# Optimization experiments

Hardware: AMD Instinct MI355X
Metric: run time of the kernel (lower is better)

## Reference

```python
import jax, jax.numpy as jnp
import numpy as np

D_MODEL = 1024
N_HEAD = 16
DH = D_MODEL // N_HEAD


def setup_inputs() -> dict:
    key = jax.random.key(0)
    ks = jax.random.split(key, 5)
    B, T = 4, 2048
    scale = 0.02
    return {
        "x": jax.random.normal(ks[0], (B, T, D_MODEL), dtype=jnp.float32),
        "Wqkv": jax.random.normal(ks[1], (D_MODEL, 3 * D_MODEL), dtype=jnp.float32) * scale,
        "bqkv": jnp.zeros((3 * D_MODEL,), dtype=jnp.float32),
        "Wout": jax.random.normal(ks[2], (D_MODEL, D_MODEL), dtype=jnp.float32) * scale,
        "bout": jnp.zeros((D_MODEL,), dtype=jnp.float32),
    }


def reference(x, Wqkv, bqkv, Wout, bout):
    B, T, C = x.shape
    qkv = x @ Wqkv + bqkv  # [B,T,3C]
    q, k, v = jnp.split(qkv, 3, axis=2)
    # [B,T,C] -> [B,H,T,dh]
    def heads(t):
        return t.reshape(B, T, N_HEAD, DH).transpose(0, 2, 1, 3)
    q, k, v = heads(q), heads(k), heads(v)
    scores = jnp.einsum("bhqd,bhkd->bhqk", q, k) / jnp.sqrt(jnp.float32(DH))
    causal = jnp.tril(jnp.ones((T, T), dtype=bool))  # [T,T]
    neg = jnp.finfo(scores.dtype).min
    scores = jnp.where(causal[None, None, :, :], scores, neg)
    A = jax.nn.softmax(scores, axis=-1)
    y = jnp.einsum("bhqk,bhkd->bhqd", A, v)
    y = y.transpose(0, 2, 1, 3).reshape(B, T, C)
    return y @ Wout + bout
```

## Files before the change

### kernel.cpp

```cpp
#include <hip/hip_runtime.h>
#include <hip/hip_bf16.h>

typedef float f32x4 __attribute__((ext_vector_type(4)));
typedef float f32x16 __attribute__((ext_vector_type(16)));
typedef short s16x8 __attribute__((ext_vector_type(8)));
typedef short s16x4 __attribute__((ext_vector_type(4)));
typedef unsigned int u32x4 __attribute__((ext_vector_type(4)));

#define B_ 4
#define T_ 2048
#define C_ 1024
#define H_ 16
#define DH_ 64
#define M_ (B_*T_)
#define N3_ (3*C_)

static __device__ __forceinline__ short f2bf(float f) {
    __hip_bfloat16 h = __float2bfloat16(f);
    return *reinterpret_cast<short*>(&h);
}

static __device__ __forceinline__ unsigned pack2(float lo, float hi) {
    unsigned r;
    asm("v_cvt_pk_bf16_f32 %0, %1, %2" : "=v"(r) : "v"(lo), "v"(hi));
    return r;
}

static __device__ __forceinline__ float exp2_raw(float x) {
    float r;
    asm("v_exp_f32 %0, %1" : "=v"(r) : "v"(x));
    return r;
}

static __device__ __forceinline__ void gload16(const void* g, void* l) {
    __builtin_amdgcn_global_load_lds(
        (const __attribute__((address_space(1))) void*)g,
        (__attribute__((address_space(3))) void*)l, 16, 0, 0);
}

static __device__ __forceinline__ s16x8 lds_frag(const short* base, int row, int chunk) {
    return *(const s16x8*)&base[(row << 6) + ((chunk ^ (row & 7)) << 3)];
}


__global__ __launch_bounds__(256) void cast_f32_bf16(
    const float* __restrict__ in, short* __restrict__ out, int n8)
{
    int i = blockIdx.x * 256 + threadIdx.x;
    if (i >= n8) return;
    float4 a = *(const float4*)&in[i * 8];
    float4 b = *(const float4*)&in[i * 8 + 4];
    s16x8 o = { f2bf(a.x), f2bf(a.y), f2bf(a.z), f2bf(a.w),
                f2bf(b.x), f2bf(b.y), f2bf(b.z), f2bf(b.w) };
    *(s16x8*)&out[i * 8] = o;
}

__global__ __launch_bounds__(256) void transpose_cast(
    const float* __restrict__ src, short* __restrict__ dst, int K, int N)
{
    __shared__ short t[64][66];
    int tid = threadIdx.x;
    int n0 = blockIdx.x * 64, k0 = blockIdx.y * 64;
    #pragma unroll
    for (int p = 0; p < 4; ++p) {
        int cid = tid + p * 256;
        int r = cid >> 4, c4 = cid & 15;
        float4 v = *(const float4*)&src[(size_t)(k0 + r) * N + n0 + c4 * 4];
        t[r][c4 * 4 + 0] = f2bf(v.x);
        t[r][c4 * 4 + 1] = f2bf(v.y);
        t[r][c4 * 4 + 2] = f2bf(v.z);
        t[r][c4 * 4 + 3] = f2bf(v.w);
    }
    __syncthreads();
    #pragma unroll
    for (int p = 0; p < 4; ++p) {
        int cid = tid + p * 256;
        int r = cid >> 4, c4 = cid & 15;
        s16x4 ov;
        #pragma unroll
        for (int j = 0; j < 4; ++j) ov[j] = t[c4 * 4 + j][r];
        *(s16x4*)&dst[(size_t)(n0 + r) * K + k0 + c4 * 4] = ov;
    }
}


template<int MODE>
__global__ __launch_bounds__(256) void gemm_bt(
    const short* __restrict__ A, const short* __restrict__ Bt,
    const float* __restrict__ bias, float* __restrict__ out,
    short* __restrict__ qout, short* __restrict__ kout, short* __restrict__ vout)
{
    const int K = 1024;
    __shared__ short As[128 * 64];
    __shared__ short Bs[128 * 64];
    int tid = threadIdx.x;
    int lane = tid & 63, w = tid >> 6;
    int d = lane & 15, g = lane >> 4;
    int wm = w >> 1, wn = w & 1;

    int gx = gridDim.x;
    int lid = blockIdx.y * gx + blockIdx.x;
    int chunk = (gx * gridDim.y) >> 3;
    int sl = (lid & 7) * chunk + (lid >> 3);
    int m0 = (sl / gx) * 128, n0 = (sl % gx) * 128;

    f32x4 acc[4][4];
    #pragma unroll
    for (int i = 0; i < 4; ++i)
        #pragma unroll
        for (int j = 0; j < 4; ++j) acc[i][j] = (f32x4){0.f, 0.f, 0.f, 0.f};

    for (int kt = 0; kt < K; kt += 64) {
        #pragma unroll
        for (int p = 0; p < 4; ++p) {
            int cid = p * 256 + tid;
            int r = cid >> 3, c8 = cid & 7;
            int co = (c8 ^ (r & 7)) << 3;
            int dofs = (p * 256 + (tid & ~63)) * 8;
            gload16(&A[(size_t)(m0 + r) * K + kt + co], &As[dofs]);
            gload16(&Bt[(size_t)(n0 + r) * K + kt + co], &Bs[dofs]);
        }
        __syncthreads();
        #pragma unroll
        for (int ks = 0; ks < 2; ++ks) {
            s16x8 af[4], bf[4];
            #pragma unroll
            for (int i = 0; i < 4; ++i) {
                af[i] = lds_frag(As, wm * 64 + i * 16 + d, ks * 4 + g);
                bf[i] = lds_frag(Bs, wn * 64 + i * 16 + d, ks * 4 + g);
            }
            #pragma unroll
            for (int mi = 0; mi < 4; ++mi)
                #pragma unroll
                for (int ni = 0; ni < 4; ++ni)
                    acc[mi][ni] = __builtin_amdgcn_mfma_f32_16x16x32_bf16(
                        af[mi], bf[ni], acc[mi][ni], 0, 0, 0);
        }
        __syncthreads();
    }

    #pragma unroll
    for (int mi = 0; mi < 4; ++mi)
        #pragma unroll
        for (int ni = 0; ni < 4; ++ni) {
            int gn = n0 + wn * 64 + ni * 16 + d;
            float bv = bias[gn];
            int gm0 = m0 + wm * 64 + mi * 16 + g * 4;
            if (MODE == 0) {
                #pragma unroll
                for (int r = 0; r < 4; ++r)
                    out[(size_t)(gm0 + r) * 1024 + gn] = acc[mi][ni][r] + bv;
            } else {
                int which = gn >> 10, cc = gn & 1023;
                int h = cc >> 6, dh = cc & 63;
                int b = gm0 >> 11;
                if (which == 2) {
                    int g2 = ((g & 1) << 1) | (g >> 1);
                    int t0v = (gm0 & 2047) - g * 4 + g2 * 4;
                    s16x4 pv;
                    #pragma unroll
                    for (int r = 0; r < 4; ++r) pv[r] = f2bf(acc[mi][ni][r] + bv);
                    *(s16x4*)&vout[((size_t)(b * 16 + h) * 64 + dh) * 2048 + t0v] = pv;
                } else if (which == 1) {
                    int t0 = gm0 & 2047;
                    #pragma unroll
                    for (int r = 0; r < 4; ++r)
                        kout[((size_t)(b * 16 + h) * 2048 + (t0 + r)) * 64 + dh] =
                            f2bf(acc[mi][ni][r] + bv);
                } else {
                    int t0 = gm0 & 2047;
                    const float SC2 = 0.125f * 1.44269504089f;
                    #pragma unroll
                    for (int r = 0; r < 4; ++r)
                        qout[((size_t)(b * 16 + h) * 2048 + (t0 + r)) * 64 + dh] =
                            f2bf((acc[mi][ni][r] + bv) * SC2);
                }
            }
        }
}


__global__ __launch_bounds__(256, 4) void attn_fwd(
    const short* __restrict__ q, const short* __restrict__ kk,
    const short* __restrict__ vt, short* __restrict__ y)
{
    __shared__ short Ks[2][64 * 64];
    __shared__ short Vs[2][64 * 64];
    int tid = threadIdx.x, w = tid >> 6;
    int lane = tid & 63;
    int q5 = lane & 31, h5 = lane >> 5;
    int bid = blockIdx.x;
    int idx = bid >> 3;
    int qt = 15 - (idx >> 3);
    int bh = ((idx & 7) << 3) | (bid & 7);
    int b = bh >> 4, hh = bh & 15;
    const size_t hb = (size_t)bh * 2048 * 64;
    int nt = 2 * qt + 2;
    int qrow = qt * 128 + w * 32;
    int qg = qrow + q5;

    s16x8 qf[4];
    #pragma unroll
    for (int s = 0; s < 4; ++s)
        qf[s] = *(const s16x8*)&q[hb + (size_t)qg * 64 + 16 * s + 8 * h5];

    f32x16 oA, oB;
    #pragma unroll
    for (int i = 0; i < 16; ++i) { oA[i] = 0.f; oB[i] = 0.f; }
    float l = 0.f;

    #define STAGE(buf, kt2) do { \
        _Pragma("unroll") \
        for (int p = 0; p < 2; ++p) { \
            int cid = p * 256 + tid; \
            int r__ = cid >> 3, c8__ = cid & 7; \
            int co__ = (c8__ ^ (r__ & 7)) << 3; \
            int dofs__ = (p * 256 + (tid & ~63)) * 8; \
            gload16(&kk[hb + (size_t)((kt2) * 64 + r__) * 64 + co__], &Ks[buf][dofs__]); \
            gload16(&vt[hb + (size_t)r__ * 2048 + (kt2) * 64 + co__], &Vs[buf][dofs__]); \
        } \
    } while (0)

    STAGE(0, 0);
    int cur = 0;

    #pragma unroll 1
    for (int t = 0; t < nt; ++t) {
        if (t + 1 < nt) {
            STAGE(cur ^ 1, t + 1);
            asm volatile("s_waitcnt vmcnt(4)" ::: "memory");
        } else {
            asm volatile("s_waitcnt vmcnt(0)" ::: "memory");
        }
        __builtin_amdgcn_s_barrier();

        if (t * 64 <= qrow + 31) {
            const short* Kb = Ks[cur];
            const short* Vb = Vs[cur];

            f32x16 sA, sB;
            #pragma unroll
            for (int i = 0; i < 16; ++i) { sA[i] = 0.f; sB[i] = 0.f; }
            #pragma unroll
            for (int s = 0; s < 4; ++s) {
                sA = __builtin_amdgcn_mfma_f32_32x32x16_bf16(
                    lds_frag(Kb, q5, 2 * s + h5), qf[s], sA, 0, 0, 0);
                sB = __builtin_amdgcn_mfma_f32_32x32x16_bf16(
                    lds_frag(Kb, 32 + q5, 2 * s + h5), qf[s], sB, 0, 0, 0);
            }

            float eA[16], eB[16];
            float S = 0.f;
            if (t * 64 + 63 > qrow) {
                #pragma unroll
                for (int rg = 0; rg < 16; ++rg) {
                    int kg = t * 64 + (rg & 3) + 8 * (rg >> 2) + 4 * h5;
                    float a = exp2_raw(sA[rg]); if (kg > qg) a = 0.f;
                    float c = exp2_raw(sB[rg]); if (kg + 32 > qg) c = 0.f;
                    eA[rg] = a; eB[rg] = c; S += a + c;
                }
            } else {
                #pragma unroll
                for (int rg = 0; rg < 16; ++rg) {
                    float a = exp2_raw(sA[rg]);
                    float c = exp2_raw(sB[rg]);
                    eA[rg] = a; eB[rg] = c; S += a + c;
                }
            }
            l += S;

            unsigned wdA[8], wdB[8];
            #pragma unroll
            for (int m = 0; m < 4; ++m) {
                wdA[2 * m]     = pack2(eA[4 * m],     eA[4 * m + 1]);
                wdA[2 * m + 1] = pack2(eA[4 * m + 2], eA[4 * m + 3]);
                wdB[2 * m]     = pack2(eB[4 * m],     eB[4 * m + 1]);
                wdB[2 * m + 1] = pack2(eB[4 * m + 2], eB[4 * m + 3]);
            }

            #pragma unroll
            for (int kc = 0; kc < 4; ++kc) {
                const unsigned* wsrc = (kc < 2) ? wdA : wdB;
                int o4 = (kc & 1) << 2;
                u32x4 pw = {wsrc[o4], wsrc[o4 + 1], wsrc[o4 + 2], wsrc[o4 + 3]};
                s16x8 pb = __builtin_bit_cast(s16x8, pw);
                oA = __builtin_amdgcn_mfma_f32_32x32x16_bf16(
                    lds_frag(Vb, q5, 2 * kc + h5), pb, oA, 0, 0, 0);
                oB = __builtin_amdgcn_mfma_f32_32x32x16_bf16(
                    lds_frag(Vb, 32 + q5, 2 * kc + h5), pb, oB, 0, 0, 0);
            }
        }

        __builtin_amdgcn_s_barrier();
        cur ^= 1;
    }

    l += __shfl_xor(l, 32);
    float rl = 1.0f / l;

    short* yp = &y[(size_t)(b * 2048 + qg) * 1024 + hh * 64];
    #pragma unroll
    for (int m = 0; m < 4; ++m) {
        s16x4 v0, v1;
        #pragma unroll
        for (int i = 0; i < 4; ++i) {
            v0[i] = f2bf(oA[4 * m + i] * rl);
            v1[i] = f2bf(oB[4 * m + i] * rl);
        }
        *(s16x4*)&yp[8 * m + 4 * h5] = v0;
        *(s16x4*)&yp[32 + 8 * m + 4 * h5] = v1;
    }
    #undef STAGE
}


extern "C" void kernel_launch(void* const* d_in, const int* in_sizes, int n_in,
                              void* d_out, int out_size, void* d_ws, size_t ws_size,
                              hipStream_t stream)
{
    const float* x    = (const float*)d_in[0];
    const float* Wqkv = (const float*)d_in[1];
    const float* bqkv = (const float*)d_in[2];
    const float* Wout = (const float*)d_in[3];
    const float* bout = (const float*)d_in[4];
    float* out = (float*)d_out;

    char* ws = (char*)d_ws;
    short* xbf   = (short*)ws;  ws += (size_t)M_ * C_ * 2;
    short* wqkvT = (short*)ws;  ws += (size_t)N3_ * C_ * 2;
    short* woutT = (short*)ws;  ws += (size_t)C_ * C_ * 2;
    short* qb    = (short*)ws;  ws += (size_t)M_ * C_ * 2;
    short* kb    = (short*)ws;  ws += (size_t)M_ * C_ * 2;
    short* vtb   = (short*)ws;  ws += (size_t)M_ * C_ * 2;
    short* yb    = (short*)ws;  ws += (size_t)M_ * C_ * 2;

    cast_f32_bf16<<<(M_ * C_ / 8 + 255) / 256, 256, 0, stream>>>(x, xbf, M_ * C_ / 8);
    transpose_cast<<<dim3(N3_ / 64, C_ / 64), 256, 0, stream>>>(Wqkv, wqkvT, C_, N3_);
    transpose_cast<<<dim3(C_ / 64, C_ / 64), 256, 0, stream>>>(Wout, woutT, C_, C_);

    gemm_bt<1><<<dim3(N3_ / 128, M_ / 128), 256, 0, stream>>>(
        xbf, wqkvT, bqkv, nullptr, qb, kb, vtb);

    attn_fwd<<<dim3((T_ / 128) * B_ * H_), 256, 0, stream>>>(qb, kb, vtb, yb);

    gemm_bt<0><<<dim3(C_ / 128, M_ / 128), 256, 0, stream>>>(
        yb, woutT, bout, out, nullptr, nullptr, nullptr);
}
```

Measured before the change: 177.6 us.

## Double-buffer GEMM LDS tiles to overlap global loads with MFMA compute

The GEMM k-loop now uses two LDS buffers for A and B. It issues the direct-to-LDS loads for the next k-tile before computing on the current one, and waits with vmcnt(8) so only the older batch has to land. The aim is to hide global-memory latency behind MFMA work instead of stalling on a full __syncthreads each iteration. The cost is double the shared memory (64KB per block), which may lower occupancy. The raw s_barrier plus manual waitcnt also carries some risk of LDS visibility hazards.

```diff
diff --git a/kernel.cpp b/kernel.cpp
--- a/kernel.cpp
+++ b/kernel.cpp
@@ -91,8 +91,8 @@
     short* __restrict__ qout, short* __restrict__ kout, short* __restrict__ vout)
 {
     const int K = 1024;
-    __shared__ short As[128 * 64];
-    __shared__ short Bs[128 * 64];
+    __shared__ short As[2][128 * 64];
+    __shared__ short Bs[2][128 * 64];
     int tid = threadIdx.x;
     int lane = tid & 63, w = tid >> 6;
     int d = lane & 15, g = lane >> 4;
@@ -110,24 +110,41 @@
         #pragma unroll
         for (int j = 0; j < 4; ++j) acc[i][j] = (f32x4){0.f, 0.f, 0.f, 0.f};
 
+    int r_ = tid >> 3, c8_ = tid & 7;
+    int co_ = (c8_ ^ (r_ & 7)) << 3;
+
+    #define GSTAGE(buf, kt) do { \
+        _Pragma("unroll") \
+        for (int p = 0; p < 4; ++p) { \
+            int rr = p * 32 + r_; \
+            int dofs = (p * 256 + (tid & ~63)) * 8; \
+            gload16(&A[(size_t)(m0 + rr) * K + (kt) + co_], &As[buf][dofs]); \
+            gload16(&Bt[(size_t)(n0 + rr) * K + (kt) + co_], &Bs[buf][dofs]); \
+        } \
+    } while (0)
+
+    GSTAGE(0, 0);
+    int cur = 0;
+
+    #pragma unroll 1
     for (int kt = 0; kt < K; kt += 64) {
-        #pragma unroll
-        for (int p = 0; p < 4; ++p) {
-            int cid = p * 256 + tid;
-            int r = cid >> 3, c8 = cid & 7;
-            int co = (c8 ^ (r & 7)) << 3;
-            int dofs = (p * 256 + (tid & ~63)) * 8;
-            gload16(&A[(size_t)(m0 + r) * K + kt + co], &As[dofs]);
-            gload16(&Bt[(size_t)(n0 + r) * K + kt + co], &Bs[dofs]);
-        }
-        __syncthreads();
+        if (kt + 64 < K) {
+            GSTAGE(cur ^ 1, kt + 64);
+            asm volatile("s_waitcnt vmcnt(8)" ::: "memory");
+        } else {
+            asm volatile("s_waitcnt vmcnt(0)" ::: "memory");
+        }
+        __builtin_amdgcn_s_barrier();
+
+        const short* Ab = As[cur];
+        const short* Bb = Bs[cur];
         #pragma unroll
         for (int ks = 0; ks < 2; ++ks) {
             s16x8 af[4], bf[4];
             #pragma unroll
             for (int i = 0; i < 4; ++i) {
-                af[i] = lds_frag(As, wm * 64 + i * 16 + d, ks * 4 + g);
-                bf[i] = lds_frag(Bs, wn * 64 + i * 16 + d, ks * 4 + g);
+                af[i] = lds_frag(Ab, wm * 64 + i * 16 + d, ks * 4 + g);
+                bf[i] = lds_frag(Bb, wn * 64 + i * 16 + d, ks * 4 + g);
             }
             #pragma unroll
             for (int mi = 0; mi < 4; ++mi)
@@ -136,8 +153,11 @@
                     acc[mi][ni] = __builtin_amdgcn_mfma_f32_16x16x32_bf16(
                         af[mi], bf[ni], acc[mi][ni], 0, 0, 0);
         }
-        __syncthreads();
-    }
+
+        __builtin_amdgcn_s_barrier();
+        cur ^= 1;
+    }
+    #undef GSTAGE
 
     #pragma unroll
     for (int mi = 0; mi < 4; ++mi)
```

Measured after the change: 171.2 us. -3.6%, faster.
